# Kernel optimization log

Measured on AMD Instinct MI355X. Metric: run time of the kernel, lower is better.

Reference implementation:

```python
import jax, jax.numpy as jnp
import numpy as np
from jax import lax

K = 3        # kernel size
PAD = 1      # padding
K2 = K * K


def conv2d(x, w, b):
    # x: [B,C,H,W], w: [O,C,K,K], b: [O]
    y = lax.conv_general_dilated(
        x, w, window_strides=(1, 1), padding=((PAD, PAD), (PAD, PAD)),
        dimension_numbers=("NCHW", "OIHW", "NCHW"))
    return y + b[None, :, None, None]


def bilinear_sample(img, py, px):
    # img: [C,H,W]; py, px: [K2,H,W] float sampling coords (zero padding outside)
    H, W = img.shape[1], img.shape[2]
    y0 = jnp.floor(py); x0 = jnp.floor(px)
    wy1 = py - y0; wx1 = px - x0
    wy0 = 1.0 - wy1; wx0 = 1.0 - wx1

    def gather(yi, xi, wgt):
        yc = jnp.clip(yi, 0, H - 1).astype(jnp.int32)
        xc = jnp.clip(xi, 0, W - 1).astype(jnp.int32)
        valid = ((yi >= 0) & (yi <= H - 1) & (xi >= 0) & (xi <= W - 1))
        v = img[:, yc, xc]                      # [C,K2,H,W]
        return v * (wgt * valid.astype(img.dtype))[None]

    return (gather(y0, x0, wy0 * wx0) + gather(y0, x0 + 1, wy0 * wx1)
            + gather(y0 + 1, x0, wy1 * wx0) + gather(y0 + 1, x0 + 1, wy1 * wx1))


def deform_conv2d(x, offset, weight, bias):
    # x: [B,C,H,W], offset: [B,2*K2,H,W] as (dy,dx) pairs per kernel tap
    B, C, H, W = x.shape
    off = offset.reshape(B, K2, 2, H, W)
    ks_y = (jnp.arange(K2) // K - PAD).astype(x.dtype)   # kernel tap y offsets
    ks_x = (jnp.arange(K2) % K - PAD).astype(x.dtype)
    base_y = ks_y[:, None, None] + jnp.arange(H, dtype=x.dtype)[None, :, None]
    base_x = ks_x[:, None, None] + jnp.arange(W, dtype=x.dtype)[None, None, :]
    py = off[:, :, 0] + base_y                            # [B,K2,H,W]
    px = off[:, :, 1] + base_x
    sampled = jax.vmap(bilinear_sample)(x, py, px)        # [B,C,K2,H,W]
    out = jnp.einsum("bckhw,ock->bohw", sampled, weight.reshape(weight.shape[0], C, K2))
    return out + bias[None, :, None, None]


def setup_inputs() -> dict:
    key = jax.random.key(0)
    ks = jax.random.split(key, 5)
    B, C, O, H, W = 4, 64, 64, 128, 128
    s_off = 1.0 / np.sqrt(C * K2)
    return {
        "x": jax.random.normal(ks[0], (B, C, H, W), dtype=jnp.float32),
        "w_off": jax.random.normal(ks[1], (2 * K2, C, K, K), dtype=jnp.float32) * s_off,
        "b_off": jnp.zeros((2 * K2,), dtype=jnp.float32),
        "weight": jax.random.normal(ks[2], (O, C, K, K), dtype=jnp.float32) * s_off,
        "bias": jax.random.normal(ks[3], (O,), dtype=jnp.float32) * 0.01,
    }


def reference(x, w_off, b_off, weight, bias):
    offset = conv2d(x, w_off, b_off)          # [B,18,H,W]
    return deform_conv2d(x, offset, weight, bias)
```

## Files before the change

kernel.cpp:

```cpp
#include <hip/hip_runtime.h>
#include <hip/hip_bf16.h>

#define BB 4
#define CC 64
#define OO 64
#define HH 128
#define WW 128
#define HW (HH * WW)
#define K2 9
#define OCOFF 18
#define SMP_STRIDE 36

typedef __attribute__((ext_vector_type(8))) short short8;
typedef __attribute__((ext_vector_type(16))) float f32x16;

union U8 { unsigned u[4]; short8 s8; };

__device__ __forceinline__ float uf(unsigned u) { return __builtin_bit_cast(float, u); }

__device__ __forceinline__ unsigned cvtpk(float a, float b) {
  unsigned r;
  asm("v_cvt_pk_bf16_f32 %0, %1, %2" : "=v"(r) : "v"(a), "v"(b));
  return r;
}
__device__ __forceinline__ void split2(float a, float b, unsigned& ph, unsigned& pl) {
  ph = cvtpk(a, b);
  float ra = a - uf(ph << 16);
  float rb = b - uf(ph & 0xFFFF0000u);
  pl = cvtpk(ra, rb);
}

__device__ __forceinline__ unsigned short bf16_rne(float v) {
  unsigned u = __builtin_bit_cast(unsigned, v);
  return (unsigned short)((u + 0x7FFFu + ((u >> 16) & 1u)) >> 16);
}
__device__ __forceinline__ void bf16_split(float v, unsigned short& hi, unsigned short& lo) {
  hi = bf16_rne(v);
  float hf = __builtin_bit_cast(float, (unsigned)hi << 16);
  lo = bf16_rne(v - hf);
}
__device__ __forceinline__ float4 ld4(const float* p) { return *(const float4*)p; }

__global__ __launch_bounds__(256) void prep_all(
    const float* __restrict__ x, const float* __restrict__ weight,
    const float* __restrict__ w_off, float* __restrict__ xt,
    unsigned* __restrict__ wf, unsigned* __restrict__ wof) {
  int blk = blockIdx.x;
  int t = threadIdx.x;
  if (blk < 2048) {
    __shared__ float tile[64][33];
    int wt = blk & 3, h = (blk >> 2) & 127, b = blk >> 9;
    int w0 = wt * 32;
    {
      int w_l = t & 31, c_l = t >> 5;
#pragma unroll
      for (int i = 0; i < 8; ++i) {
        int cc = c_l * 8 + i;
        tile[cc][w_l] = x[(((size_t)b * 64 + cc) * 128 + h) * 128 + w0 + w_l];
      }
    }
    __syncthreads();
    {
      int c_w = t & 63, w_w = t >> 6;
#pragma unroll
      for (int i = 0; i < 8; ++i) {
        int wl = w_w * 8 + i;
        xt[(((size_t)b * 128 + h) * 128 + w0 + wl) * 64 + c_w] = tile[c_w][wl];
      }
    }
    return;
  }
  if (blk < 2048 + 144) {
    int d = (blk - 2048) * 256 + t;
    if (d >= 9 * 4096) return;
    int j2 = d & 3, l = (d >> 2) & 63, hh = (d >> 8) & 1, s = (d >> 9) & 3,
        m = (d >> 11) & 1, c = d >> 12;
    int o = m * 32 + (l & 31);
    int g = l >> 5;
    int ch0 = s * 16 + g * 8 + j2 * 2;
    float v0 = weight[(o * 64 + ch0) * 9 + c];
    float v1 = weight[(o * 64 + ch0 + 1) * 9 + c];
    unsigned short h0, l0, h1, l1;
    bf16_split(v0, h0, l0);
    bf16_split(v1, h1, l1);
    unsigned short b0 = hh ? l0 : h0;
    unsigned short b1 = hh ? l1 : h1;
    wf[d] = (unsigned)b0 | ((unsigned)b1 << 16);
    return;
  }
  {
    int d = (blk - 2192) * 256 + t;
    if (d >= 9 * 2048) return;
    int j2 = d & 3, l = (d >> 2) & 63, hh = (d >> 8) & 1, s = (d >> 9) & 3,
        c = d >> 11;
    int oc = l & 31;
    int g = l >> 5;
    int ch0 = s * 16 + g * 8 + j2 * 2;
    unsigned r = 0;
    if (oc < OCOFF) {
      float v0 = w_off[(oc * 64 + ch0) * 9 + c];
      float v1 = w_off[(oc * 64 + ch0 + 1) * 9 + c];
      unsigned short h0, l0, h1, l1;
      bf16_split(v0, h0, l0);
      bf16_split(v1, h1, l1);
      unsigned short b0 = hh ? l0 : h0;
      unsigned short b1 = hh ? l1 : h1;
      r = (unsigned)b0 | ((unsigned)b1 << 16);
    }
    wof[d] = r;
    return;
  }
}

struct TapD { int o00, o01, o10, o11; float w00, w01, w10, w11; };

__device__ __forceinline__ TapD mk_tapd(float oyv, float oxv, int h, int wpix, int kk) {
  TapD t;
  const int dy = kk / 3 - 1, dx = kk - (kk / 3) * 3 - 1;
  float py = oyv + (float)(h + dy);
  float px = oxv + (float)(wpix + dx);
  float y0f = floorf(py), x0f = floorf(px);
  float wy1 = py - y0f, wx1 = px - x0f;
  float wy0 = 1.0f - wy1, wx0 = 1.0f - wx1;
  int y0 = (int)y0f, x0 = (int)x0f, y1 = y0 + 1, x1 = x0 + 1;
  bool vy0 = (unsigned)y0 < (unsigned)HH, vy1 = (unsigned)y1 < (unsigned)HH;
  bool vx0 = (unsigned)x0 < (unsigned)WW, vx1 = (unsigned)x1 < (unsigned)WW;
  t.w00 = (vy0 && vx0) ? wy0 * wx0 : 0.0f;
  t.w01 = (vy0 && vx1) ? wy0 * wx1 : 0.0f;
  t.w10 = (vy1 && vx0) ? wy1 * wx0 : 0.0f;
  t.w11 = (vy1 && vx1) ? wy1 * wx1 : 0.0f;
  int y0c = min(max(y0, 0), HH - 1), y1c = min(max(y1, 0), HH - 1);
  int x0c = min(max(x0, 0), WW - 1), x1c = min(max(x1, 0), WW - 1);
  t.o00 = (y0c * WW + x0c) * CC;
  t.o01 = (y0c * WW + x1c) * CC;
  t.o10 = (y1c * WW + x0c) * CC;
  t.o11 = (y1c * WW + x1c) * CC;
  return t;
}

__device__ __forceinline__ void issueD(float4 (&st)[8], const float* xb,
                                       const TapD& t, int j4) {
  st[0] = ld4(xb + t.o00 + j4);      st[1] = ld4(xb + t.o01 + j4);
  st[2] = ld4(xb + t.o10 + j4);      st[3] = ld4(xb + t.o11 + j4);
  st[4] = ld4(xb + t.o00 + 32 + j4); st[5] = ld4(xb + t.o01 + 32 + j4);
  st[6] = ld4(xb + t.o10 + 32 + j4); st[7] = ld4(xb + t.o11 + 32 + j4);
}

__device__ __forceinline__ void consumeD(unsigned* mh, unsigned* ml,
                                         int pl, int j,
                                         const float4 (&st)[8], const TapD& t) {
#pragma unroll
  for (int hf = 0; hf < 2; ++hf) {
    float v[4];
#pragma unroll
    for (int q = 0; q < 4; ++q)
      v[q] = fmaf(t.w00, st[hf * 4 + 0][q], fmaf(t.w01, st[hf * 4 + 1][q],
             fmaf(t.w10, st[hf * 4 + 2][q], t.w11 * st[hf * 4 + 3][q])));
    unsigned h01, l01, h23, l23;
    split2(v[0], v[1], h01, l01);
    split2(v[2], v[3], h23, l23);
    int idx = pl * SMP_STRIDE + hf * 16 + j * 2;
    *(uint2*)&mh[idx] = make_uint2(h01, h23);
    *(uint2*)&ml[idx] = make_uint2(l01, l23);
  }
}

__global__ __launch_bounds__(128, 2) void fused_deform(
    const float* __restrict__ xt, const unsigned* __restrict__ wfrag,
    const unsigned* __restrict__ wofrag, const float* __restrict__ b_off,
    const float* __restrict__ bias, float* __restrict__ out) {
  __shared__ __align__(16) unsigned smph[2][32 * SMP_STRIDE];
  __shared__ __align__(16) unsigned smpl[2][32 * SMP_STRIDE];
  __shared__ __align__(16) float offs_lds[2][32 * OCOFF];

  const int blk = blockIdx.x;
  const int sx = (blk & 7) * 128 + (blk >> 3);
  const int seg = sx & 1, h = (sx >> 1) & 127, b = sx >> 8;
  const int tid = threadIdx.x;
  const int l = tid & 63, wv = tid >> 6;
  const int P = l & 31, g = l >> 5;
  const int j = l & 7, pq = l >> 3;
  const int j4 = j * 4;
  const int wbase = seg * 64 + wv * 32;

  const float* xb = xt + (size_t)b * HW * CC;
  unsigned* mh = smph[wv];
  unsigned* ml = smpl[wv];
  float* ol = offs_lds[wv];

  {
    f32x16 accO = {0,0,0,0,0,0,0,0,0,0,0,0,0,0,0,0};
#pragma unroll
    for (int c = 0; c < 9; ++c) {
      const int dy = c / 3 - 1, dx = c - (c / 3) * 3 - 1;
      const int y = h + dy;
      const int xp = wbase + P + dx;
      const bool valid = ((unsigned)y < (unsigned)HH) && ((unsigned)xp < (unsigned)WW);
      const unsigned msk = valid ? 0xFFFFFFFFu : 0u;
      const int yc = min(max(y, 0), HH - 1), xc = min(max(xp, 0), WW - 1);
      const unsigned* rowp = (const unsigned*)(xb + (size_t)(yc * WW + xc) * CC);
#pragma unroll
      for (int s = 0; s < 4; ++s) {
        const int cb = s * 16 + g * 8;
        uint4 u0 = *(const uint4*)(rowp + cb);
        uint4 u1 = *(const uint4*)(rowp + cb + 4);
        u0.x &= msk; u0.y &= msk; u0.z &= msk; u0.w &= msk;
        u1.x &= msk; u1.y &= msk; u1.z &= msk; u1.w &= msk;
        U8 sh, sl;
        split2(uf(u0.x), uf(u0.y), sh.u[0], sl.u[0]);
        split2(uf(u0.z), uf(u0.w), sh.u[1], sl.u[1]);
        split2(uf(u1.x), uf(u1.y), sh.u[2], sl.u[2]);
        split2(uf(u1.z), uf(u1.w), sh.u[3], sl.u[3]);
        const unsigned* wb = wofrag + ((size_t)((c * 8 + s * 2) * 64 + l)) * 4;
        short8 wh = *(const short8*)(wb);
        short8 wl = *(const short8*)(wb + 256);
        accO = __builtin_amdgcn_mfma_f32_32x32x16_bf16(wh, sh.s8, accO, 0, 0, 0);
        accO = __builtin_amdgcn_mfma_f32_32x32x16_bf16(wh, sl.s8, accO, 0, 0, 0);
        accO = __builtin_amdgcn_mfma_f32_32x32x16_bf16(wl, sh.s8, accO, 0, 0, 0);
      }
    }
#pragma unroll
    for (int r = 0; r < 16; ++r) {
      int oc = (r & 3) + 8 * (r >> 2) + 4 * g;
      if (oc < OCOFF) ol[P * OCOFF + oc] = accO[r] + b_off[oc];
    }
  }

  f32x16 acc0 = {0,0,0,0,0,0,0,0,0,0,0,0,0,0,0,0};
  f32x16 acc1 = {0,0,0,0,0,0,0,0,0,0,0,0,0,0,0,0};
  {
    TapD tA, tB;
    float4 sA[8], sB[8];
    {
      float2 o = *(const float2*)&ol[pq * OCOFF + 0];
      tA = mk_tapd(o.x, o.y, h, wbase + pq, 0);
      issueD(sA, xb, tA, j4);
    }
#pragma unroll
    for (int c = 0; c < 9; ++c) {
      {
        float2 o = *(const float2*)&ol[(8 + pq) * OCOFF + 2 * c];
        tB = mk_tapd(o.x, o.y, h, wbase + 8 + pq, c);
        issueD(sB, xb, tB, j4);
      }
      consumeD(mh, ml, pq, j, sA, tA);
      {
        float2 o = *(const float2*)&ol[(16 + pq) * OCOFF + 2 * c];
        tA = mk_tapd(o.x, o.y, h, wbase + 16 + pq, c);
        issueD(sA, xb, tA, j4);
      }
      consumeD(mh, ml, 8 + pq, j, sB, tB);
      {
        float2 o = *(const float2*)&ol[(24 + pq) * OCOFF + 2 * c];
        tB = mk_tapd(o.x, o.y, h, wbase + 24 + pq, c);
        issueD(sB, xb, tB, j4);
      }
      consumeD(mh, ml, 16 + pq, j, sA, tA);
      if (c < 8) {
        float2 o = *(const float2*)&ol[pq * OCOFF + 2 * (c + 1)];
        tA = mk_tapd(o.x, o.y, h, wbase + pq, c + 1);
        issueD(sA, xb, tA, j4);
      }
      consumeD(mh, ml, 24 + pq, j, sB, tB);
#pragma unroll
      for (int s = 0; s < 4; ++s) {
        int ridx = P * SMP_STRIDE + s * 8 + g * 4;
        short8 sh8 = *(const short8*)&mh[ridx];
        short8 sl8 = *(const short8*)&ml[ridx];
        const unsigned* wb = wfrag + ((size_t)((c * 16 + s * 2) * 64 + l)) * 4;
        short8 wh0 = *(const short8*)(wb);
        short8 wl0 = *(const short8*)(wb + 256);
        short8 wh1 = *(const short8*)(wb + 2048);
        short8 wl1 = *(const short8*)(wb + 2304);
        acc0 = __builtin_amdgcn_mfma_f32_32x32x16_bf16(wh0, sh8, acc0, 0, 0, 0);
        acc0 = __builtin_amdgcn_mfma_f32_32x32x16_bf16(wh0, sl8, acc0, 0, 0, 0);
        acc0 = __builtin_amdgcn_mfma_f32_32x32x16_bf16(wl0, sh8, acc0, 0, 0, 0);
        acc1 = __builtin_amdgcn_mfma_f32_32x32x16_bf16(wh1, sh8, acc1, 0, 0, 0);
        acc1 = __builtin_amdgcn_mfma_f32_32x32x16_bf16(wh1, sl8, acc1, 0, 0, 0);
        acc1 = __builtin_amdgcn_mfma_f32_32x32x16_bf16(wl1, sh8, acc1, 0, 0, 0);
      }
    }
  }

  const int wpix = wbase + P;
#pragma unroll
  for (int r = 0; r < 16; ++r) {
    int o0 = (r & 3) + 8 * (r >> 2) + 4 * g;
    out[(((size_t)b * 64 + o0) * 128 + h) * 128 + wpix] = acc0[r] + bias[o0];
    out[(((size_t)b * 64 + 32 + o0) * 128 + h) * 128 + wpix] = acc1[r] + bias[32 + o0];
  }
}

extern "C" void kernel_launch(void* const* d_in, const int* in_sizes, int n_in,
                              void* d_out, int out_size, void* d_ws, size_t ws_size,
                              hipStream_t stream) {
  const float* x      = (const float*)d_in[0];
  const float* w_off  = (const float*)d_in[1];
  const float* b_off  = (const float*)d_in[2];
  const float* weight = (const float*)d_in[3];
  const float* bias   = (const float*)d_in[4];
  float* out = (float*)d_out;

  float*    xt     = (float*)d_ws;
  unsigned* wfrag  = (unsigned*)(xt + (size_t)4194304);
  unsigned* wofrag = wfrag + 36864;

  prep_all<<<2264, 256, 0, stream>>>(x, weight, w_off, xt, wfrag, wofrag);
  fused_deform<<<1024, 128, 0, stream>>>(xt, wfrag, wofrag, b_off, bias, out);
}
```

Measured before the change: 146.5 us.

## Deepen gather prefetch pipeline and add sched barriers and MFMA priority

The offset-conv phase now prefetches the next tap's input rows into a double-buffered register set while the current tap's MFMAs run. The deformable gather phase goes from two to four in-flight stage buffers, with sched_barrier fences to keep the load-issue order fixed. s_setprio is raised around MFMA blocks. The aim is to hide global-load latency behind compute, at the cost of more VGPRs, which risks spills or lower occupancy under the 128x2 launch bounds.

After: 136.1 us. 7.1% less time.

```diff
diff --git a/kernel.cpp b/kernel.cpp
--- a/kernel.cpp
+++ b/kernel.cpp
@@ -113,6 +113,7 @@
 }
 
 struct TapD { int o00, o01, o10, o11; float w00, w01, w10, w11; };
+struct TapW { float w00, w01, w10, w11; };
 
 __device__ __forceinline__ TapD mk_tapd(float oyv, float oxv, int h, int wpix, int kk) {
   TapD t;
@@ -138,17 +139,22 @@
   return t;
 }
 
-__device__ __forceinline__ void issueD(float4 (&st)[8], const float* xb,
-                                       const TapD& t, int j4) {
+__device__ __forceinline__ TapW stageD2(float4 (&st)[8], const float* xb,
+                                        const float* ol, int h, int wbase,
+                                        int pq, int j4, int r, int c) {
+  float2 o = *(const float2*)&ol[(r * 8 + pq) * OCOFF + 2 * c];
+  TapD t = mk_tapd(o.x, o.y, h, wbase + r * 8 + pq, c);
   st[0] = ld4(xb + t.o00 + j4);      st[1] = ld4(xb + t.o01 + j4);
   st[2] = ld4(xb + t.o10 + j4);      st[3] = ld4(xb + t.o11 + j4);
   st[4] = ld4(xb + t.o00 + 32 + j4); st[5] = ld4(xb + t.o01 + 32 + j4);
   st[6] = ld4(xb + t.o10 + 32 + j4); st[7] = ld4(xb + t.o11 + 32 + j4);
-}
-
-__device__ __forceinline__ void consumeD(unsigned* mh, unsigned* ml,
-                                         int pl, int j,
-                                         const float4 (&st)[8], const TapD& t) {
+  TapW w = { t.w00, t.w01, t.w10, t.w11 };
+  return w;
+}
+
+__device__ __forceinline__ void consD(unsigned* mh, unsigned* ml,
+                                      int pl, int j,
+                                      const float4 (&st)[8], const TapW& t) {
 #pragma unroll
   for (int hf = 0; hf < 2; ++hf) {
     float v[4];
@@ -165,6 +171,101 @@
   }
 }
 
+__device__ __forceinline__ void p2_mfma(f32x16& acc0, f32x16& acc1,
+                                        const unsigned* mh, const unsigned* ml,
+                                        const unsigned* wfrag,
+                                        int P, int g, int l, int c) {
+  __builtin_amdgcn_s_setprio(1);
+#pragma unroll
+  for (int s = 0; s < 4; ++s) {
+    int ridx = P * SMP_STRIDE + s * 8 + g * 4;
+    short8 sh8 = *(const short8*)&mh[ridx];
+    short8 sl8 = *(const short8*)&ml[ridx];
+    const unsigned* wb = wfrag + ((size_t)((c * 16 + s * 2) * 64 + l)) * 4;
+    short8 wh0 = *(const short8*)(wb);
+    short8 wl0 = *(const short8*)(wb + 256);
+    short8 wh1 = *(const short8*)(wb + 2048);
+    short8 wl1 = *(const short8*)(wb + 2304);
+    acc0 = __builtin_amdgcn_mfma_f32_32x32x16_bf16(wh0, sh8, acc0, 0, 0, 0);
+    acc0 = __builtin_amdgcn_mfma_f32_32x32x16_bf16(wh0, sl8, acc0, 0, 0, 0);
+    acc0 = __builtin_amdgcn_mfma_f32_32x32x16_bf16(wl0, sh8, acc0, 0, 0, 0);
+    acc1 = __builtin_amdgcn_mfma_f32_32x32x16_bf16(wh1, sh8, acc1, 0, 0, 0);
+    acc1 = __builtin_amdgcn_mfma_f32_32x32x16_bf16(wh1, sl8, acc1, 0, 0, 0);
+    acc1 = __builtin_amdgcn_mfma_f32_32x32x16_bf16(wl1, sh8, acc1, 0, 0, 0);
+  }
+  __builtin_amdgcn_s_setprio(0);
+}
+
+__device__ __forceinline__ unsigned stageO1(uint4 (&T)[8], const float* xb,
+                                            int h, int wP, int g, int c) {
+  const int dy = c / 3 - 1, dx = c - (c / 3) * 3 - 1;
+  const int y = h + dy, xp = wP + dx;
+  bool valid = ((unsigned)y < (unsigned)HH) && ((unsigned)xp < (unsigned)WW);
+  int yc = min(max(y, 0), HH - 1), xc = min(max(xp, 0), WW - 1);
+  const uint4* rowp = (const uint4*)(xb + (size_t)(yc * WW + xc) * CC);
+#pragma unroll
+  for (int s = 0; s < 4; ++s) {
+    T[2 * s]     = rowp[s * 4 + g * 2];
+    T[2 * s + 1] = rowp[s * 4 + g * 2 + 1];
+  }
+  return valid ? 0xFFFFFFFFu : 0u;
+}
+
+__device__ __forceinline__ void p1_tap(f32x16& accO, uint4 (&TC)[8], unsigned mskC,
+                                       uint4 (&TN)[8], unsigned& mskN,
+                                       const float* xb, const unsigned* wofrag,
+                                       int h, int wP, int g, int l, int c, bool last) {
+  if (!last) {
+    mskN = stageO1(TN, xb, h, wP, g, c + 1);
+    __builtin_amdgcn_sched_barrier(0);
+  }
+#pragma unroll
+  for (int s = 0; s < 4; ++s) {
+    uint4 u0 = TC[2 * s], u1 = TC[2 * s + 1];
+    u0.x &= mskC; u0.y &= mskC; u0.z &= mskC; u0.w &= mskC;
+    u1.x &= mskC; u1.y &= mskC; u1.z &= mskC; u1.w &= mskC;
+    U8 sh, sl;
+    split2(uf(u0.x), uf(u0.y), sh.u[0], sl.u[0]);
+    split2(uf(u0.z), uf(u0.w), sh.u[1], sl.u[1]);
+    split2(uf(u1.x), uf(u1.y), sh.u[2], sl.u[2]);
+    split2(uf(u1.z), uf(u1.w), sh.u[3], sl.u[3]);
+    const unsigned* wb = wofrag + ((size_t)((c * 8 + s * 2) * 64 + l)) * 4;
+    short8 wh = *(const short8*)(wb);
+    short8 wl = *(const short8*)(wb + 256);
+    __builtin_amdgcn_s_setprio(1);
+    accO = __builtin_amdgcn_mfma_f32_32x32x16_bf16(wh, sh.s8, accO, 0, 0, 0);
+    accO = __builtin_amdgcn_mfma_f32_32x32x16_bf16(wh, sl.s8, accO, 0, 0, 0);
+    accO = __builtin_amdgcn_mfma_f32_32x32x16_bf16(wl, sh.s8, accO, 0, 0, 0);
+    __builtin_amdgcn_s_setprio(0);
+  }
+}
+
+__device__ __forceinline__ void p2_tap(
+    f32x16& acc0, f32x16& acc1,
+    float4 (&S0)[8], float4 (&S1)[8], float4 (&S2)[8], float4 (&S3)[8],
+    TapW& t0, TapW& t1, TapW& t2, TapW& t3,
+    unsigned* mh, unsigned* ml, const float* xb, const float* ol,
+    const unsigned* wfrag, int h, int wbase, int pq, int j, int j4,
+    int P, int g, int l, int c, bool last) {
+  t2 = stageD2(S2, xb, ol, h, wbase, pq, j4, 2, c);
+  __builtin_amdgcn_sched_barrier(0);
+  consD(mh, ml, 0 * 8 + pq, j, S0, t0);
+  t3 = stageD2(S3, xb, ol, h, wbase, pq, j4, 3, c);
+  __builtin_amdgcn_sched_barrier(0);
+  consD(mh, ml, 1 * 8 + pq, j, S1, t1);
+  if (!last) {
+    t0 = stageD2(S0, xb, ol, h, wbase, pq, j4, 0, c + 1);
+    __builtin_amdgcn_sched_barrier(0);
+  }
+  consD(mh, ml, 2 * 8 + pq, j, S2, t2);
+  if (!last) {
+    t1 = stageD2(S1, xb, ol, h, wbase, pq, j4, 1, c + 1);
+    __builtin_amdgcn_sched_barrier(0);
+  }
+  consD(mh, ml, 3 * 8 + pq, j, S3, t3);
+  p2_mfma(acc0, acc1, mh, ml, wfrag, P, g, l, c);
+}
+
 __global__ __launch_bounds__(128, 2) void fused_deform(
     const float* __restrict__ xt, const unsigned* __restrict__ wfrag,
     const unsigned* __restrict__ wofrag, const float* __restrict__ b_off,
@@ -190,35 +291,19 @@
 
   {
     f32x16 accO = {0,0,0,0,0,0,0,0,0,0,0,0,0,0,0,0};
-#pragma unroll
-    for (int c = 0; c < 9; ++c) {
-      const int dy = c / 3 - 1, dx = c - (c / 3) * 3 - 1;
-      const int y = h + dy;
-      const int xp = wbase + P + dx;
-      const bool valid = ((unsigned)y < (unsigned)HH) && ((unsigned)xp < (unsigned)WW);
-      const unsigned msk = valid ? 0xFFFFFFFFu : 0u;
-      const int yc = min(max(y, 0), HH - 1), xc = min(max(xp, 0), WW - 1);
-      const unsigned* rowp = (const unsigned*)(xb + (size_t)(yc * WW + xc) * CC);
-#pragma unroll
-      for (int s = 0; s < 4; ++s) {
-        const int cb = s * 16 + g * 8;
-        uint4 u0 = *(const uint4*)(rowp + cb);
-        uint4 u1 = *(const uint4*)(rowp + cb + 4);
-        u0.x &= msk; u0.y &= msk; u0.z &= msk; u0.w &= msk;
-        u1.x &= msk; u1.y &= msk; u1.z &= msk; u1.w &= msk;
-        U8 sh, sl;
-        split2(uf(u0.x), uf(u0.y), sh.u[0], sl.u[0]);
-        split2(uf(u0.z), uf(u0.w), sh.u[1], sl.u[1]);
-        split2(uf(u1.x), uf(u1.y), sh.u[2], sl.u[2]);
-        split2(uf(u1.z), uf(u1.w), sh.u[3], sl.u[3]);
-        const unsigned* wb = wofrag + ((size_t)((c * 8 + s * 2) * 64 + l)) * 4;
-        short8 wh = *(const short8*)(wb);
-        short8 wl = *(const short8*)(wb + 256);
-        accO = __builtin_amdgcn_mfma_f32_32x32x16_bf16(wh, sh.s8, accO, 0, 0, 0);
-        accO = __builtin_amdgcn_mfma_f32_32x32x16_bf16(wh, sl.s8, accO, 0, 0, 0);
-        accO = __builtin_amdgcn_mfma_f32_32x32x16_bf16(wl, sh.s8, accO, 0, 0, 0);
-      }
-    }
+    uint4 TA[8], TB[8];
+    unsigned mskA = 0, mskB = 0;
+    mskA = stageO1(TA, xb, h, wbase + P, g, 0);
+    __builtin_amdgcn_sched_barrier(0);
+    p1_tap(accO, TA, mskA, TB, mskB, xb, wofrag, h, wbase + P, g, l, 0, false);
+    p1_tap(accO, TB, mskB, TA, mskA, xb, wofrag, h, wbase + P, g, l, 1, false);
+    p1_tap(accO, TA, mskA, TB, mskB, xb, wofrag, h, wbase + P, g, l, 2, false);
+    p1_tap(accO, TB, mskB, TA, mskA, xb, wofrag, h, wbase + P, g, l, 3, false);
+    p1_tap(accO, TA, mskA, TB, mskB, xb, wofrag, h, wbase + P, g, l, 4, false);
+    p1_tap(accO, TB, mskB, TA, mskA, xb, wofrag, h, wbase + P, g, l, 5, false);
+    p1_tap(accO, TA, mskA, TB, mskB, xb, wofrag, h, wbase + P, g, l, 6, false);
+    p1_tap(accO, TB, mskB, TA, mskA, xb, wofrag, h, wbase + P, g, l, 7, false);
+    p1_tap(accO, TA, mskA, TB, mskB, xb, wofrag, h, wbase + P, g, l, 8, true);
 #pragma unroll
     for (int r = 0; r < 16; ++r) {
       int oc = (r & 3) + 8 * (r >> 2) + 4 * g;
@@ -229,57 +314,30 @@
   f32x16 acc0 = {0,0,0,0,0,0,0,0,0,0,0,0,0,0,0,0};
   f32x16 acc1 = {0,0,0,0,0,0,0,0,0,0,0,0,0,0,0,0};
   {
-    TapD tA, tB;
-    float4 sA[8], sB[8];
-    {
-      float2 o = *(const float2*)&ol[pq * OCOFF + 0];
-      tA = mk_tapd(o.x, o.y, h, wbase + pq, 0);
-      issueD(sA, xb, tA, j4);
-    }
-#pragma unroll
-    for (int c = 0; c < 9; ++c) {
-      {
-        float2 o = *(const float2*)&ol[(8 + pq) * OCOFF + 2 * c];
-        tB = mk_tapd(o.x, o.y, h, wbase + 8 + pq, c);
-        issueD(sB, xb, tB, j4);
-      }
-      consumeD(mh, ml, pq, j, sA, tA);
-      {
-        float2 o = *(const float2*)&ol[(16 + pq) * OCOFF + 2 * c];
-        tA = mk_tapd(o.x, o.y, h, wbase + 16 + pq, c);
-        issueD(sA, xb, tA, j4);
-      }
-      consumeD(mh, ml, 8 + pq, j, sB, tB);
-      {
-        float2 o = *(const float2*)&ol[(24 + pq) * OCOFF + 2 * c];
-        tB = mk_tapd(o.x, o.y, h, wbase + 24 + pq, c);
-        issueD(sB, xb, tB, j4);
-      }
-      consumeD(mh, ml, 16 + pq, j, sA, tA);
-      if (c < 8) {
-        float2 o = *(const float2*)&ol[pq * OCOFF + 2 * (c + 1)];
-        tA = mk_tapd(o.x, o.y, h, wbase + pq, c + 1);
-        issueD(sA, xb, tA, j4);
-      }
-      consumeD(mh, ml, 24 + pq, j, sB, tB);
-#pragma unroll
-      for (int s = 0; s < 4; ++s) {
-        int ridx = P * SMP_STRIDE + s * 8 + g * 4;
-        short8 sh8 = *(const short8*)&mh[ridx];
-        short8 sl8 = *(const short8*)&ml[ridx];
-        const unsigned* wb = wfrag + ((size_t)((c * 16 + s * 2) * 64 + l)) * 4;
-        short8 wh0 = *(const short8*)(wb);
-        short8 wl0 = *(const short8*)(wb + 256);
-        short8 wh1 = *(const short8*)(wb + 2048);
-        short8 wl1 = *(const short8*)(wb + 2304);
-        acc0 = __builtin_amdgcn_mfma_f32_32x32x16_bf16(wh0, sh8, acc0, 0, 0, 0);
-        acc0 = __builtin_amdgcn_mfma_f32_32x32x16_bf16(wh0, sl8, acc0, 0, 0, 0);
-        acc0 = __builtin_amdgcn_mfma_f32_32x32x16_bf16(wl0, sh8, acc0, 0, 0, 0);
-        acc1 = __builtin_amdgcn_mfma_f32_32x32x16_bf16(wh1, sh8, acc1, 0, 0, 0);
-        acc1 = __builtin_amdgcn_mfma_f32_32x32x16_bf16(wh1, sl8, acc1, 0, 0, 0);
-        acc1 = __builtin_amdgcn_mfma_f32_32x32x16_bf16(wl1, sh8, acc1, 0, 0, 0);
-      }
-    }
+    float4 S0[8], S1[8], S2[8], S3[8];
+    TapW t0, t1, t2, t3;
+    t0 = stageD2(S0, xb, ol, h, wbase, pq, j4, 0, 0);
+    __builtin_amdgcn_sched_barrier(0);
+    t1 = stageD2(S1, xb, ol, h, wbase, pq, j4, 1, 0);
+    __builtin_amdgcn_sched_barrier(0);
+    p2_tap(acc0, acc1, S0, S1, S2, S3, t0, t1, t2, t3, mh, ml, xb, ol, wfrag,
+           h, wbase, pq, j, j4, P, g, l, 0, false);
+    p2_tap(acc0, acc1, S0, S1, S2, S3, t0, t1, t2, t3, mh, ml, xb, ol, wfrag,
+           h, wbase, pq, j, j4, P, g, l, 1, false);
+    p2_tap(acc0, acc1, S0, S1, S2, S3, t0, t1, t2, t3, mh, ml, xb, ol, wfrag,
+           h, wbase, pq, j, j4, P, g, l, 2, false);
+    p2_tap(acc0, acc1, S0, S1, S2, S3, t0, t1, t2, t3, mh, ml, xb, ol, wfrag,
+           h, wbase, pq, j, j4, P, g, l, 3, false);
+    p2_tap(acc0, acc1, S0, S1, S2, S3, t0, t1, t2, t3, mh, ml, xb, ol, wfrag,
+           h, wbase, pq, j, j4, P, g, l, 4, false);
+    p2_tap(acc0, acc1, S0, S1, S2, S3, t0, t1, t2, t3, mh, ml, xb, ol, wfrag,
+           h, wbase, pq, j, j4, P, g, l, 5, false);
+    p2_tap(acc0, acc1, S0, S1, S2, S3, t0, t1, t2, t3, mh, ml, xb, ol, wfrag,
+           h, wbase, pq, j, j4, P, g, l, 6, false);
+    p2_tap(acc0, acc1, S0, S1, S2, S3, t0, t1, t2, t3, mh, ml, xb, ol, wfrag,
+           h, wbase, pq, j, j4, P, g, l, 7, false);
+    p2_tap(acc0, acc1, S0, S1, S2, S3, t0, t1, t2, t3, mh, ml, xb, ol, wfrag,
+           h, wbase, pq, j, j4, P, g, l, 8, true);
   }
 
   const int wpix = wbase + P;
```
